# Kernel tuning notes

Measured on AMD Instinct MI355X. Metric: run time of the kernel, lower is better.

The kernel has to match this reference:

```python
import jax, jax.numpy as jnp
import numpy as np

N = 100000      # nodes
E = 1600000     # edges
IN = 256        # in_channels
H = 128         # hidden_channels
OUT = 64        # output_channels
B = 64          # graphs in batch
EPS = 1e-5      # BatchNorm eps


def setup_inputs() -> dict:
    key = jax.random.key(0)
    ks = jax.random.split(key, 32)

    def lin_w(k, fan_in, fan_out):
        return (jax.random.normal(k, (fan_in, fan_out), jnp.float32) / np.sqrt(fan_in)).astype(jnp.float32)

    inp = {
        'x': jax.random.normal(ks[0], (N, IN), jnp.float32),
        'edge_index': jax.random.randint(ks[1], (2, E), 0, N, dtype=jnp.int32),
        'batch': jnp.sort(jax.random.randint(ks[2], (N,), 0, B, dtype=jnp.int32)),
        # GCN conv weights (layer 0: IN->H, layers 1,2: H->H)
        'W0': lin_w(ks[3], IN, H), 'b0': jnp.zeros((H,), jnp.float32),
        'W1': lin_w(ks[4], H, H),  'b1': jnp.zeros((H,), jnp.float32),
        'W2': lin_w(ks[5], H, H),  'b2': jnp.zeros((H,), jnp.float32),
        # BatchNorm affine params per layer
        'g0': 1.0 + 0.1 * jax.random.normal(ks[6], (H,), jnp.float32),
        'be0': 0.1 * jax.random.normal(ks[7], (H,), jnp.float32),
        'g1': 1.0 + 0.1 * jax.random.normal(ks[8], (H,), jnp.float32),
        'be1': 0.1 * jax.random.normal(ks[9], (H,), jnp.float32),
        'g2': 1.0 + 0.1 * jax.random.normal(ks[10], (H,), jnp.float32),
        'be2': 0.1 * jax.random.normal(ks[11], (H,), jnp.float32),
        # residual projection (in_channels != hidden_channels)
        'Wres': lin_w(ks[12], IN, H), 'bres': jnp.zeros((H,), jnp.float32),
        # head MLP: Linear(H,H) -> ReLU -> Dropout(eval) -> Linear(H,OUT)
        'Wl0': lin_w(ks[13], H, H), 'bl0': jnp.zeros((H,), jnp.float32),
        'Wl1': lin_w(ks[14], H, OUT), 'bl1': jnp.zeros((OUT,), jnp.float32),
    }
    return inp


def _gcn_layer(h, src, dst, dinv, W, b):
    # PyG GCNConv: linear first, then sym-normalized aggregation with self loops
    h = h @ W                                   # [N, d_out]
    enorm = dinv[src] * dinv[dst]               # [E]
    msg = h[src] * enorm[:, None]               # gather + scale  [E, d_out]
    agg = jax.ops.segment_sum(msg, dst, num_segments=N)
    agg = agg + h * (dinv * dinv)[:, None]      # self-loop contribution (norm = 1/deg)
    return agg + b


def _bn_eval(h, g, be):
    # inference BatchNorm with running_mean=0, running_var=1
    return h * (g / np.sqrt(1.0 + EPS)) + be


def reference(x, edge_index, batch,
              W0, b0, W1, b1, W2, b2,
              g0, be0, g1, be1, g2, be2,
              Wres, bres, Wl0, bl0, Wl1, bl1):
    src, dst = edge_index[0], edge_index[1]
    # degrees with self loops (edge weight 1)
    deg = jax.ops.segment_sum(jnp.ones((E,), jnp.float32), dst, num_segments=N) + 1.0
    dinv = jax.lax.rsqrt(deg)                   # [N]

    Ws, bs, gs, bes = [W0, W1, W2], [b0, b1, b2], [g0, g1, g2], [be0, be1, be2]
    h = x
    for i in range(3):
        h = _gcn_layer(h, src, dst, dinv, Ws[i], bs[i])
        h = jax.nn.relu(_bn_eval(h, gs[i], bes[i]))  # dropout is identity in eval
        if i == 0:
            h = h + (x @ Wres + bres)           # residual projection of original input

    # head MLP on node features
    out = jax.nn.relu(h @ Wl0 + bl0) @ Wl1 + bl1    # [N, OUT]

    # global mean pool over graphs
    counts = jax.ops.segment_sum(jnp.ones((N,), jnp.float32), batch, num_segments=B)
    pooled = jax.ops.segment_sum(h, batch, num_segments=B) / jnp.maximum(counts, 1.0)[:, None]
    return out, pooled
```

## Files before the change

kernel.cpp:

```cpp
#include <hip/hip_runtime.h>
#include <hip/hip_fp16.h>

typedef __half f16;
typedef _Float16 half8 __attribute__((ext_vector_type(8)));
typedef float floatx4 __attribute__((ext_vector_type(4)));

#define NN   100000
#define NE   1600000
#define CIN  256
#define CH   128
#define COUT 64
#define NB   64

#define NBUK 128
#define NPB  782
#define BCAP 32
#define CAPB 20480
#define G1   512
#define EPB  3125
#define CSZ  15104

__global__ void k_sentinel(float* __restrict__ out, int n, float val) {
    int i = blockIdx.x * 256 + threadIdx.x;
    if (i < n) out[i] = val;
}

__global__ void k_init(float* __restrict__ pool, float* __restrict__ cnt,
                       int* __restrict__ gcur) {
    int i = blockIdx.x * 256 + threadIdx.x;
    if (i < NB * CH) pool[i] = 0.0f;
    if (i < NB) cnt[i] = 0.0f;
    if (i < NBUK) gcur[i] = i * CAPB;
}

__global__ __launch_bounds__(256) void k_bin(const int* __restrict__ src,
                                             const int* __restrict__ dst,
                                             int* __restrict__ gcur,
                                             int* __restrict__ stage) {
    __shared__ int bins[NBUK][BCAP];
    __shared__ int bcnt[NBUK];
    __shared__ int fcnt[NBUK];
    __shared__ int fbase[NBUK];
    const int tid = threadIdx.x;
    if (tid < NBUK) bcnt[tid] = 0;
    __syncthreads();
    const int e0 = blockIdx.x * EPB;
    const int e1 = (e0 + EPB < NE) ? e0 + EPB : NE;
    for (int base = e0; base < e1; base += 256) {
        int e = base + tid;
        if (e < e1) {
            int s = src[e], d = dst[e];
            int bk = d / NPB;
            int pk = ((d - bk * NPB) << 17) | s;
            int pos = atomicAdd(&bcnt[bk], 1);
            if (pos < BCAP) {
                bins[bk][pos] = pk;
            } else {
                int gp = atomicAdd(&gcur[bk], 1);
                if (gp < (bk + 1) * CAPB) stage[gp] = pk;
            }
        }
        __syncthreads();
        if (tid < NBUK) {
            int stored = bcnt[tid]; if (stored > BCAP) stored = BCAP;
            int nf = stored & ~15;
            fcnt[tid] = nf;
            if (nf) fbase[tid] = atomicAdd(&gcur[tid], nf);
        }
        __syncthreads();
#pragma unroll
        for (int pass = 0; pass < NBUK / 16; ++pass) {
            int b = pass * 16 + (tid >> 4);
            int sl = tid & 15;
            int nf = fcnt[b];
            int fb = fbase[b];
            for (int k = sl; k < nf; k += 16)
                if (fb + k < (b + 1) * CAPB) stage[fb + k] = bins[b][k];
        }
        __syncthreads();
        if (tid < NBUK) {
            int stored = bcnt[tid]; if (stored > BCAP) stored = BCAP;
            int nf = fcnt[tid];
            for (int k = nf; k < stored; ++k) bins[tid][k - nf] = bins[tid][k];
            bcnt[tid] = stored - nf;
        }
        __syncthreads();
    }
    if (tid < NBUK) {
        int stored = bcnt[tid];
        fcnt[tid] = stored;
        if (stored) fbase[tid] = atomicAdd(&gcur[tid], stored);
    }
    __syncthreads();
#pragma unroll
    for (int pass = 0; pass < NBUK / 16; ++pass) {
        int b = pass * 16 + (tid >> 4);
        int sl = tid & 15;
        int nf = fcnt[b];
        int fb = fbase[b];
        for (int k = sl; k < nf; k += 16)
            if (fb + k < (b + 1) * CAPB) stage[fb + k] = bins[b][k];
    }
}

__global__ void k_gtot(const int* __restrict__ gcur, int* __restrict__ barr,
                       int* __restrict__ rowptr) {
    int lane = threadIdx.x;
    int carry = 0;
    for (int c0 = 0; c0 < NBUK; c0 += 64) {
        int idx = c0 + lane;
        int orig = gcur[idx] - idx * CAPB;
        int v = orig;
#pragma unroll
        for (int off = 1; off < 64; off <<= 1) {
            int t = __shfl_up(v, off);
            if (lane >= off) v += t;
        }
        barr[idx] = v - orig + carry;
        carry += __shfl(v, 63);
    }
    if (lane == 0) rowptr[NN] = NE;
}

__global__ __launch_bounds__(256) void k_csr(const int* __restrict__ gcur,
                                             const int* __restrict__ barr,
                                             const int* __restrict__ stage,
                                             int* __restrict__ rowptr,
                                             int* __restrict__ csr,
                                             float* __restrict__ dinv) {
    __shared__ int hist[NPB];
    __shared__ int lcsr[CSZ];
    const int b = blockIdx.x, tid = threadIdx.x;
    const int nbase = b * NPB;
    const int nloc = (NPB < NN - nbase) ? NPB : NN - nbase;
    const int count = gcur[b] - b * CAPB;
    const int gbase = barr[b];
    const int sb = b * CAPB;
    for (int i = tid; i < NPB; i += 256) hist[i] = 0;
    __syncthreads();
    for (int i = tid; i < count; i += 256)
        atomicAdd(&hist[stage[sb + i] >> 17], 1);
    __syncthreads();
    for (int dl = tid; dl < nloc; dl += 256)
        dinv[nbase + dl] = rsqrtf((float)hist[dl] + 1.0f);
    __syncthreads();
    if (tid < 64) {
        int carry = 0;
        for (int c0 = 0; c0 < NPB; c0 += 64) {
            int idx = c0 + tid;
            int orig = (idx < NPB) ? hist[idx] : 0;
            int v = orig;
#pragma unroll
            for (int off = 1; off < 64; off <<= 1) {
                int t = __shfl_up(v, off);
                if (tid >= off) v += t;
            }
            if (idx < NPB) hist[idx] = v - orig + carry;
            carry += __shfl(v, 63);
        }
    }
    __syncthreads();
    for (int dl = tid; dl < nloc; dl += 256)
        rowptr[nbase + dl] = gbase + hist[dl];
    __syncthreads();
    const bool fits = (count <= CSZ);
    for (int i = tid; i < count; i += 256) {
        int pk = stage[sb + i];
        int dl = pk >> 17, s = pk & 0x1FFFF;
        int pos = atomicAdd(&hist[dl], 1);
        if (fits) lcsr[pos] = s;
        else csr[gbase + pos] = s;
    }
    __syncthreads();
    if (fits)
        for (int i = tid; i < count; i += 256) csr[gbase + i] = lcsr[i];
}

__global__ __launch_bounds__(256) void k_wconv(
        const float* __restrict__ W0, const float* __restrict__ Wres,
        const float* __restrict__ W1, const float* __restrict__ W2,
        const float* __restrict__ Wl0, const float* __restrict__ Wl1,
        half8* __restrict__ F0, half8* __restrict__ Fres,
        half8* __restrict__ F1, half8* __restrict__ F2,
        half8* __restrict__ Fl0, half8* __restrict__ Fl1) {
    int f = blockIdx.x * 256 + threadIdx.x;
    const float* W; half8* F; int M, base;
    if      (f <  4096) { W = W0;   F = F0;   M = 128; base = 0; }
    else if (f <  8192) { W = Wres; F = Fres; M = 128; base = 4096; }
    else if (f < 10240) { W = W1;   F = F1;   M = 128; base = 8192; }
    else if (f < 12288) { W = W2;   F = F2;   M = 128; base = 10240; }
    else if (f < 14336) { W = Wl0;  F = Fl0;  M = 128; base = 12288; }
    else if (f < 15360) { W = Wl1;  F = Fl1;  M = 64;  base = 14336; }
    else return;
    int fl = f - base;
    int lane = fl & 63, fm = lane & 15, g = lane >> 4;
    int rest = fl >> 6;
    int nt = M / 16;
    int t = rest % nt, kt = rest / nt;
    half8 v;
#pragma unroll
    for (int j = 0; j < 8; ++j)
        v[j] = (_Float16)W[(size_t)(kt * 32 + g * 8 + j) * M + t * 16 + fm];
    F[fl] = v;
}

__global__ __launch_bounds__(256) void k_mfma0(const float* __restrict__ x,
                                               const half8* __restrict__ WF,
                                               const half8* __restrict__ WFb,
                                               const float* __restrict__ bres,
                                               const float* __restrict__ dinv,
                                               f16* __restrict__ lout,
                                               f16* __restrict__ rout) {
    constexpr int APAD = 40;
    __shared__ __align__(16) _Float16 Al[2][64 * APAD];
    __shared__ __align__(16) _Float16 Bl[2][16 * 512];
    const int tid = threadIdx.x;
    const int wave = tid >> 6, lane = tid & 63;
    const int fm = lane & 15, g = lane >> 4;
    const int rb = blockIdx.x * 64;

    const int arow = tid >> 2;
    const int koff = (tid & 3) * 8;
    const int grow = rb + arow;
    const bool live = (grow < NN);
    const float* xp = x + (size_t)(live ? grow : 0) * CIN + koff;

    const int bt = wave * 4;

    floatx4 acc[16];
#pragma unroll
    for (int t = 0; t < 16; ++t)
#pragma unroll
        for (int r = 0; r < 4; ++r) acc[t][r] = 0.0f;

    float4 a0, a1;
    half8 rB[4];

    auto ldA = [&](int kt) {
        if (live) {
            a0 = *(const float4*)(xp + kt * 32);
            a1 = *(const float4*)(xp + kt * 32 + 4);
        } else {
            a0 = make_float4(0.f, 0.f, 0.f, 0.f);
            a1 = make_float4(0.f, 0.f, 0.f, 0.f);
        }
    };
    auto ldB = [&](int kt) {
#pragma unroll
        for (int i = 0; i < 4; ++i) {
            int t = bt + i;
            rB[i] = (t < 8) ? WF[((size_t)kt * 8 + t) * 64 + lane]
                            : WFb[((size_t)kt * 8 + (t - 8)) * 64 + lane];
        }
    };
    auto stA = [&](int buf) {
        half8 h;
        h[0] = (_Float16)a0.x; h[1] = (_Float16)a0.y;
        h[2] = (_Float16)a0.z; h[3] = (_Float16)a0.w;
        h[4] = (_Float16)a1.x; h[5] = (_Float16)a1.y;
        h[6] = (_Float16)a1.z; h[7] = (_Float16)a1.w;
        *(half8*)&Al[buf][arow * APAD + koff] = h;
    };
    auto stB = [&](int buf) {
#pragma unroll
        for (int i = 0; i < 4; ++i)
            *(half8*)&Bl[buf][(bt + i) * 512 + lane * 8] = rB[i];
    };

    ldA(0); ldB(0);
    stA(0); stB(0);
    __syncthreads();

    for (int kt = 0; kt < 8; ++kt) {
        const int cur = kt & 1;
        if (kt < 7) { ldA(kt + 1); ldB(kt + 1); }
        half8 afrag = *(const half8*)&Al[cur][(wave * 16 + fm) * APAD + g * 8];
#pragma unroll
        for (int t = 0; t < 8; ++t) {
            half8 bfrag = *(const half8*)&Bl[cur][t * 512 + lane * 8];
            acc[t] = __builtin_amdgcn_mfma_f32_16x16x32_f16(afrag, bfrag, acc[t], 0, 0, 0);
        }
#pragma unroll
        for (int t = 0; t < 8; ++t) {
            half8 bfrag = *(const half8*)&Bl[cur][(8 + t) * 512 + lane * 8];
            acc[8 + t] = __builtin_amdgcn_mfma_f32_16x16x32_f16(afrag, bfrag, acc[8 + t], 0, 0, 0);
        }
        if (kt < 7) { stA(cur ^ 1); stB(cur ^ 1); }
        __syncthreads();
    }

    const int rloc = wave * 16 + g * 4;
#pragma unroll
    for (int t = 0; t < 8; ++t) {
        int col = t * 16 + fm;
#pragma unroll
        for (int r = 0; r < 4; ++r) {
            int row = rb + rloc + r;
            if (row < NN) lout[(size_t)row * 128 + col] = (f16)(acc[t][r] * dinv[row]);
        }
    }
#pragma unroll
    for (int t = 0; t < 8; ++t) {
        int col = t * 16 + fm;
        float bb = bres[col];
#pragma unroll
        for (int r = 0; r < 4; ++r) {
            int row = rb + rloc + r;
            if (row < NN) rout[(size_t)row * 128 + col] = (f16)(acc[8 + t][r] + bb);
        }
    }
}

__global__ __launch_bounds__(256) void k_lin(const f16* __restrict__ A,
                                             const half8* __restrict__ WF,
                                             const float* __restrict__ dinv,
                                             f16* __restrict__ lout) {
    const int tid = threadIdx.x;
    const int wave = tid >> 6, lane = tid & 63;
    const int fm = lane & 15, g = lane >> 4;
    const int tb = blockIdx.x * 64 + wave * 16;
    const int arow = tb + fm;

    half8 af[4];
#pragma unroll
    for (int kt = 0; kt < 4; ++kt) {
        if (arow < NN) {
            af[kt] = *(const half8*)((const _Float16*)A + (size_t)arow * CH + kt * 32 + g * 8);
        } else {
#pragma unroll
            for (int i = 0; i < 8; ++i) af[kt][i] = (_Float16)0.0f;
        }
    }

    floatx4 acc[8];
#pragma unroll
    for (int t = 0; t < 8; ++t)
#pragma unroll
        for (int r = 0; r < 4; ++r) acc[t][r] = 0.0f;

#pragma unroll
    for (int kt = 0; kt < 4; ++kt)
#pragma unroll
        for (int t = 0; t < 8; ++t)
            acc[t] = __builtin_amdgcn_mfma_f32_16x16x32_f16(
                af[kt], WF[((size_t)kt * 8 + t) * 64 + lane], acc[t], 0, 0, 0);

#pragma unroll
    for (int t = 0; t < 8; ++t) {
        int col = t * 16 + fm;
#pragma unroll
        for (int r = 0; r < 4; ++r) {
            int row = tb + g * 4 + r;
            if (row < NN) lout[(size_t)row * CH + col] = (f16)(acc[t][r] * dinv[row]);
        }
    }
}

__global__ __launch_bounds__(256) void k_head(const f16* __restrict__ A,
                                              const half8* __restrict__ WF0,
                                              const half8* __restrict__ WF1,
                                              const float* __restrict__ bl0,
                                              const float* __restrict__ bl1,
                                              float* __restrict__ outp) {
    constexpr int LP = 136;
    __shared__ __align__(16) _Float16 Hs[64 * LP];
    const int tid = threadIdx.x;
    const int wave = tid >> 6, lane = tid & 63;
    const int fm = lane & 15, g = lane >> 4;
    const int tb = blockIdx.x * 64 + wave * 16;
    const int arow = tb + fm;

    half8 af[4];
#pragma unroll
    for (int kt = 0; kt < 4; ++kt) {
        if (arow < NN) {
            af[kt] = *(const half8*)((const _Float16*)A + (size_t)arow * CH + kt * 32 + g * 8);
        } else {
#pragma unroll
            for (int i = 0; i < 8; ++i) af[kt][i] = (_Float16)0.0f;
        }
    }

    floatx4 acc[8];
#pragma unroll
    for (int t = 0; t < 8; ++t)
#pragma unroll
        for (int r = 0; r < 4; ++r) acc[t][r] = 0.0f;

#pragma unroll
    for (int kt = 0; kt < 4; ++kt)
#pragma unroll
        for (int t = 0; t < 8; ++t)
            acc[t] = __builtin_amdgcn_mfma_f32_16x16x32_f16(
                af[kt], WF0[((size_t)kt * 8 + t) * 64 + lane], acc[t], 0, 0, 0);

    const int lrow = wave * 16 + g * 4;
#pragma unroll
    for (int t = 0; t < 8; ++t) {
        int col = t * 16 + fm;
        float b = bl0[col];
#pragma unroll
        for (int r = 0; r < 4; ++r)
            Hs[(lrow + r) * LP + col] = (_Float16)fmaxf(acc[t][r] + b, 0.0f);
    }
    __syncthreads();

    floatx4 acc2[4];
#pragma unroll
    for (int t = 0; t < 4; ++t)
#pragma unroll
        for (int r = 0; r < 4; ++r) acc2[t][r] = 0.0f;

#pragma unroll
    for (int kt = 0; kt < 4; ++kt) {
        half8 a2 = *(const half8*)&Hs[(wave * 16 + fm) * LP + kt * 32 + g * 8];
#pragma unroll
        for (int t = 0; t < 4; ++t)
            acc2[t] = __builtin_amdgcn_mfma_f32_16x16x32_f16(
                a2, WF1[((size_t)kt * 4 + t) * 64 + lane], acc2[t], 0, 0, 0);
    }

#pragma unroll
    for (int t = 0; t < 4; ++t) {
        int col = t * 16 + fm;
        float b = bl1[col];
#pragma unroll
        for (int r = 0; r < 4; ++r) {
            int row = tb + g * 4 + r;
            if (row < NN) outp[(size_t)row * COUT + col] = acc2[t][r] + b;
        }
    }
}

template <bool RES>
__global__ __launch_bounds__(256) void k_gather(const int* __restrict__ rowptr,
                                                const int* __restrict__ csr,
                                                const float* __restrict__ dinv,
                                                const f16* __restrict__ lin,
                                                const f16* __restrict__ res,
                                                f16* __restrict__ h,
                                                const float* __restrict__ b,
                                                const float* __restrict__ g,
                                                const float* __restrict__ be) {
    const int gw = (blockIdx.x * 256 + threadIdx.x) >> 6;
    const int lane = threadIdx.x & 63;
    if (gw >= NN) return;
    const __half2* lp = (const __half2*)lin;
    const int start = __builtin_amdgcn_readfirstlane(rowptr[gw]);
    const int end   = __builtin_amdgcn_readfirstlane(rowptr[gw + 1]);

    float2 acc = __half22float2(lp[(size_t)gw * 64 + lane]);
    int j = start;
    for (; j + 7 < end; j += 8) {
        int s0 = csr[j],     s1 = csr[j + 1], s2 = csr[j + 2], s3 = csr[j + 3];
        int s4 = csr[j + 4], s5 = csr[j + 5], s6 = csr[j + 6], s7 = csr[j + 7];
        float2 v0 = __half22float2(lp[(size_t)s0 * 64 + lane]);
        float2 v1 = __half22float2(lp[(size_t)s1 * 64 + lane]);
        float2 v2 = __half22float2(lp[(size_t)s2 * 64 + lane]);
        float2 v3 = __half22float2(lp[(size_t)s3 * 64 + lane]);
        float2 v4 = __half22float2(lp[(size_t)s4 * 64 + lane]);
        float2 v5 = __half22float2(lp[(size_t)s5 * 64 + lane]);
        float2 v6 = __half22float2(lp[(size_t)s6 * 64 + lane]);
        float2 v7 = __half22float2(lp[(size_t)s7 * 64 + lane]);
        acc.x += ((v0.x + v1.x) + (v2.x + v3.x)) + ((v4.x + v5.x) + (v6.x + v7.x));
        acc.y += ((v0.y + v1.y) + (v2.y + v3.y)) + ((v4.y + v5.y) + (v6.y + v7.y));
    }
    for (; j + 3 < end; j += 4) {
        int s0 = csr[j], s1 = csr[j + 1], s2 = csr[j + 2], s3 = csr[j + 3];
        float2 v0 = __half22float2(lp[(size_t)s0 * 64 + lane]);
        float2 v1 = __half22float2(lp[(size_t)s1 * 64 + lane]);
        float2 v2 = __half22float2(lp[(size_t)s2 * 64 + lane]);
        float2 v3 = __half22float2(lp[(size_t)s3 * 64 + lane]);
        acc.x += (v0.x + v1.x) + (v2.x + v3.x);
        acc.y += (v0.y + v1.y) + (v2.y + v3.y);
    }
    for (; j < end; ++j) {
        int s = csr[j];
        float2 v = __half22float2(lp[(size_t)s * 64 + lane]);
        acc.x += v.x;
        acc.y += v.y;
    }
    const float inv_sqrt = 0.99999500003749968f;
    float dv = dinv[gw];
    int f = lane * 2;
    float2 bb = *(const float2*)&b[f];
    float2 gg = *(const float2*)&g[f];
    float2 ee = *(const float2*)&be[f];
    float t0 = fmaxf((acc.x * dv + bb.x) * (gg.x * inv_sqrt) + ee.x, 0.0f);
    float t1 = fmaxf((acc.y * dv + bb.y) * (gg.y * inv_sqrt) + ee.y, 0.0f);
    if (RES) {
        float2 rv = __half22float2(((const __half2*)res)[(size_t)gw * 64 + lane]);
        t0 += rv.x;
        t1 += rv.y;
    }
    ((__half2*)h)[(size_t)gw * 64 + lane] = __floats2half2_rn(t0, t1);
}

__global__ void k_count(const int* __restrict__ batch, float* __restrict__ cnt) {
    __shared__ float hist[NB];
    int tid = threadIdx.x;
    if (tid < NB) hist[tid] = 0.0f;
    __syncthreads();
    int n = blockIdx.x * 256 + tid;
    if (n < NN) atomicAdd(&hist[batch[n]], 1.0f);
    __syncthreads();
    if (tid < NB && hist[tid] != 0.0f) atomicAdd(&cnt[tid], hist[tid]);
}

__global__ void k_pool(const f16* __restrict__ h, const int* __restrict__ batch,
                       float* __restrict__ pool) {
    int n0 = blockIdx.x * 64;
    int j = threadIdx.x;
    int cur = batch[n0];
    float acc = 0.0f;
    int nend = (n0 + 64 < NN) ? n0 + 64 : NN;
    for (int n = n0; n < nend; ++n) {
        int b = batch[n];
        if (b != cur) {
            atomicAdd(&pool[cur * CH + j], acc);
            acc = 0.0f;
            cur = b;
        }
        acc += (float)h[(size_t)n * CH + j];
    }
    atomicAdd(&pool[cur * CH + j], acc);
}

__global__ void k_pool_fin(const float* __restrict__ pool,
                           const float* __restrict__ cnt,
                           float* __restrict__ out) {
    int i = blockIdx.x * 256 + threadIdx.x;
    if (i < NB * CH) {
        float c = fmaxf(cnt[i / CH], 1.0f);
        out[i] = pool[i] / c;
    }
}

extern "C" void kernel_launch(void* const* d_in, const int* in_sizes, int n_in,
                              void* d_out, int out_size, void* d_ws, size_t ws_size,
                              hipStream_t stream) {
    float* outp  = (float*)d_out;
    float* poolp = outp + (size_t)NN * COUT;

    const size_t HB = (size_t)NN * CH * 2;
    const size_t LB = (size_t)NN * CH * 2;
    const size_t RB = (size_t)NN * CH * 2;
    const size_t DV = (size_t)NN * 4;
    const size_t RP = 400016;
    const size_t CS = (size_t)NE * 4;
    const size_t GC = 512;
    const size_t BA = 528;
    const size_t PL = (size_t)NB * CH * 4;
    const size_t CT = 256;
    const size_t F0B = 4096 * 16, F1B = 2048 * 16, FLB = 1024 * 16;
    const size_t need = HB + LB + RB + DV + RP + CS + GC + BA + PL + CT
                        + 2 * F0B + 3 * F1B + FLB;
    if (ws_size < need) {
        k_sentinel<<<(out_size + 255) / 256, 256, 0, stream>>>(outp, out_size, 2000.0f);
        return;
    }
    char* p = (char*)d_ws;
    f16*   hbuf   = (f16*)p;               p += HB;
    f16*   lbuf   = (f16*)p;               p += LB;
    f16*   rbuf   = (f16*)p;
    int*   stage  = (int*)p;               p += RB;
    float* dinv   = (float*)p;             p += DV;
    int*   rowptr = (int*)p;               p += RP;
    int*   csr    = (int*)p;               p += CS;
    int*   gcur   = (int*)p;               p += GC;
    int*   barr   = (int*)p;               p += BA;
    float* pool   = (float*)p;             p += PL;
    float* cnt    = (float*)p;             p += CT;
    half8* F0     = (half8*)p;             p += F0B;
    half8* Fres   = (half8*)p;             p += F0B;
    half8* F1     = (half8*)p;             p += F1B;
    half8* F2     = (half8*)p;             p += F1B;
    half8* Fl0    = (half8*)p;             p += F1B;
    half8* Fl1    = (half8*)p;

    const float* x   = (const float*)d_in[0];
    const int*   ei  = (const int*)d_in[1];
    const int*   bat = (const int*)d_in[2];
    const float* W0 = (const float*)d_in[3],  *b0 = (const float*)d_in[4];
    const float* W1 = (const float*)d_in[5],  *b1 = (const float*)d_in[6];
    const float* W2 = (const float*)d_in[7],  *b2 = (const float*)d_in[8];
    const float* g0 = (const float*)d_in[9],  *be0 = (const float*)d_in[10];
    const float* g1 = (const float*)d_in[11], *be1 = (const float*)d_in[12];
    const float* g2 = (const float*)d_in[13], *be2 = (const float*)d_in[14];
    const float* Wres = (const float*)d_in[15], *bres = (const float*)d_in[16];
    const float* Wl0 = (const float*)d_in[17], *bl0 = (const float*)d_in[18];
    const float* Wl1 = (const float*)d_in[19], *bl1 = (const float*)d_in[20];

    const int* src = ei;
    const int* dst = ei + NE;

    const int gRow = (NN + 63) / 64;
    const int gGat = (NN * 64) / 256;

    k_init<<<33, 256, 0, stream>>>(pool, cnt, gcur);
    k_wconv<<<60, 256, 0, stream>>>(W0, Wres, W1, W2, Wl0, Wl1,
                                    F0, Fres, F1, F2, Fl0, Fl1);
    k_bin<<<G1, 256, 0, stream>>>(src, dst, gcur, stage);
    k_gtot<<<1, 64, 0, stream>>>(gcur, barr, rowptr);
    k_csr<<<NBUK, 256, 0, stream>>>(gcur, barr, stage, rowptr, csr, dinv);

    k_mfma0<<<gRow, 256, 0, stream>>>(x, F0, Fres, bres, dinv, lbuf, rbuf);
    k_gather<true><<<gGat, 256, 0, stream>>>(rowptr, csr, dinv, lbuf, rbuf, hbuf, b0, g0, be0);

    k_lin<<<gRow, 256, 0, stream>>>(hbuf, F1, dinv, lbuf);
    k_gather<false><<<gGat, 256, 0, stream>>>(rowptr, csr, dinv, lbuf, nullptr, hbuf, b1, g1, be1);

    k_lin<<<gRow, 256, 0, stream>>>(hbuf, F2, dinv, lbuf);
    k_gather<false><<<gGat, 256, 0, stream>>>(rowptr, csr, dinv, lbuf, nullptr, hbuf, b2, g2, be2);

    k_count<<<(NN + 255) / 256, 256, 0, stream>>>(bat, cnt);
    k_pool<<<gRow, 128, 0, stream>>>(hbuf, bat, pool);
    k_pool_fin<<<(NB * CH + 255) / 256, 256, 0, stream>>>(pool, cnt, poolp);

    k_head<<<gRow, 256, 0, stream>>>(hbuf, Fl0, Fl1, bl0, bl1, outp);
}
```

Before: 640.1 us.

## Build CSR with global atomic degree count and atomic-cursor fill instead of bucket binning

Replaces the two-pass bucket-binning CSR construction (shared-memory bins, staging buffer, per-bucket local sort) with a plain counting sort. Degrees come from global atomics, a per-bucket sum and scan produce row pointers, and edges are scattered into the CSR through global atomic cursors. This removes the staging buffer traffic and the heavy shared-memory bin management, at the cost of many contended global atomics and random scattered writes. The resulting per-row neighbor order is nondeterministic, which could change the locality of the later gathers.

```diff
diff --git a/kernel.cpp b/kernel.cpp
--- a/kernel.cpp
+++ b/kernel.cpp
@@ -14,11 +14,6 @@
 
 #define NBUK 128
 #define NPB  782
-#define BCAP 32
-#define CAPB 20480
-#define G1   512
-#define EPB  3125
-#define CSZ  15104
 
 __global__ void k_sentinel(float* __restrict__ out, int n, float val) {
     int i = blockIdx.x * 256 + threadIdx.x;
@@ -26,90 +21,47 @@
 }
 
 __global__ void k_init(float* __restrict__ pool, float* __restrict__ cnt,
-                       int* __restrict__ gcur) {
+                       int* __restrict__ deg) {
     int i = blockIdx.x * 256 + threadIdx.x;
     if (i < NB * CH) pool[i] = 0.0f;
     if (i < NB) cnt[i] = 0.0f;
-    if (i < NBUK) gcur[i] = i * CAPB;
-}
-
-__global__ __launch_bounds__(256) void k_bin(const int* __restrict__ src,
-                                             const int* __restrict__ dst,
-                                             int* __restrict__ gcur,
-                                             int* __restrict__ stage) {
-    __shared__ int bins[NBUK][BCAP];
-    __shared__ int bcnt[NBUK];
-    __shared__ int fcnt[NBUK];
-    __shared__ int fbase[NBUK];
-    const int tid = threadIdx.x;
-    if (tid < NBUK) bcnt[tid] = 0;
-    __syncthreads();
-    const int e0 = blockIdx.x * EPB;
-    const int e1 = (e0 + EPB < NE) ? e0 + EPB : NE;
-    for (int base = e0; base < e1; base += 256) {
-        int e = base + tid;
-        if (e < e1) {
-            int s = src[e], d = dst[e];
-            int bk = d / NPB;
-            int pk = ((d - bk * NPB) << 17) | s;
-            int pos = atomicAdd(&bcnt[bk], 1);
-            if (pos < BCAP) {
-                bins[bk][pos] = pk;
-            } else {
-                int gp = atomicAdd(&gcur[bk], 1);
-                if (gp < (bk + 1) * CAPB) stage[gp] = pk;
-            }
-        }
-        __syncthreads();
-        if (tid < NBUK) {
-            int stored = bcnt[tid]; if (stored > BCAP) stored = BCAP;
-            int nf = stored & ~15;
-            fcnt[tid] = nf;
-            if (nf) fbase[tid] = atomicAdd(&gcur[tid], nf);
-        }
-        __syncthreads();
-#pragma unroll
-        for (int pass = 0; pass < NBUK / 16; ++pass) {
-            int b = pass * 16 + (tid >> 4);
-            int sl = tid & 15;
-            int nf = fcnt[b];
-            int fb = fbase[b];
-            for (int k = sl; k < nf; k += 16)
-                if (fb + k < (b + 1) * CAPB) stage[fb + k] = bins[b][k];
-        }
-        __syncthreads();
-        if (tid < NBUK) {
-            int stored = bcnt[tid]; if (stored > BCAP) stored = BCAP;
-            int nf = fcnt[tid];
-            for (int k = nf; k < stored; ++k) bins[tid][k - nf] = bins[tid][k];
-            bcnt[tid] = stored - nf;
-        }
-        __syncthreads();
-    }
-    if (tid < NBUK) {
-        int stored = bcnt[tid];
-        fcnt[tid] = stored;
-        if (stored) fbase[tid] = atomicAdd(&gcur[tid], stored);
-    }
-    __syncthreads();
-#pragma unroll
-    for (int pass = 0; pass < NBUK / 16; ++pass) {
-        int b = pass * 16 + (tid >> 4);
-        int sl = tid & 15;
-        int nf = fcnt[b];
-        int fb = fbase[b];
-        for (int k = sl; k < nf; k += 16)
-            if (fb + k < (b + 1) * CAPB) stage[fb + k] = bins[b][k];
-    }
-}
-
-__global__ void k_gtot(const int* __restrict__ gcur, int* __restrict__ barr,
-                       int* __restrict__ rowptr) {
+    if (i < NN) deg[i] = 0;
+}
+
+__global__ __launch_bounds__(256) void k_deg(const int* __restrict__ dst,
+                                             int* __restrict__ deg) {
+    int i = blockIdx.x * 256 + threadIdx.x;
+    if (i < NE / 4) {
+        int4 d = ((const int4*)dst)[i];
+        atomicAdd(&deg[d.x], 1);
+        atomicAdd(&deg[d.y], 1);
+        atomicAdd(&deg[d.z], 1);
+        atomicAdd(&deg[d.w], 1);
+    }
+}
+
+__global__ __launch_bounds__(256) void k_bsum(const int* __restrict__ deg,
+                                              int* __restrict__ bsum) {
+    __shared__ int red[4];
+    const int b = blockIdx.x, tid = threadIdx.x;
+    const int nbase = b * NPB;
+    const int nend = (nbase + NPB < NN) ? nbase + NPB : NN;
+    int s = 0;
+    for (int i = nbase + tid; i < nend; i += 256) s += deg[i];
+#pragma unroll
+    for (int off = 32; off; off >>= 1) s += __shfl_down(s, off);
+    if ((tid & 63) == 0) red[tid >> 6] = s;
+    __syncthreads();
+    if (tid == 0) bsum[b] = red[0] + red[1] + red[2] + red[3];
+}
+
+__global__ void k_scanb(const int* __restrict__ bsum, int* __restrict__ barr,
+                        int* __restrict__ rowptr) {
     int lane = threadIdx.x;
     int carry = 0;
     for (int c0 = 0; c0 < NBUK; c0 += 64) {
         int idx = c0 + lane;
-        int orig = gcur[idx] - idx * CAPB;
+        int orig = bsum[idx];
         int v = orig;
 #pragma unroll
         for (int off = 1; off < 64; off <<= 1) {
@@ -122,24 +74,16 @@
     if (lane == 0) rowptr[NN] = NE;
 }
 
-__global__ __launch_bounds__(256) void k_csr(const int* __restrict__ gcur,
-                                             const int* __restrict__ barr,
-                                             const int* __restrict__ stage,
-                                             int* __restrict__ rowptr,
-                                             int* __restrict__ csr,
-                                             float* __restrict__ dinv) {
+__global__ __launch_bounds__(256) void k_brow(const int* __restrict__ deg,
+                                              const int* __restrict__ barr,
+                                              int* __restrict__ rowptr,
+                                              int* __restrict__ cursor,
+                                              float* __restrict__ dinv) {
     __shared__ int hist[NPB];
-    __shared__ int lcsr[CSZ];
     const int b = blockIdx.x, tid = threadIdx.x;
     const int nbase = b * NPB;
     const int nloc = (NPB < NN - nbase) ? NPB : NN - nbase;
-    const int count = gcur[b] - b * CAPB;
-    const int gbase = barr[b];
-    const int sb = b * CAPB;
-    for (int i = tid; i < NPB; i += 256) hist[i] = 0;
-    __syncthreads();
-    for (int i = tid; i < count; i += 256)
-        atomicAdd(&hist[stage[sb + i] >> 17], 1);
+    for (int i = tid; i < nloc; i += 256) hist[i] = deg[nbase + i];
     __syncthreads();
     for (int dl = tid; dl < nloc; dl += 256)
         dinv[nbase + dl] = rsqrtf((float)hist[dl] + 1.0f);
@@ -148,7 +92,7 @@
         int carry = 0;
         for (int c0 = 0; c0 < NPB; c0 += 64) {
             int idx = c0 + tid;
-            int orig = (idx < NPB) ? hist[idx] : 0;
+            int orig = (idx < nloc) ? hist[idx] : 0;
             int v = orig;
 #pragma unroll
             for (int off = 1; off < 64; off <<= 1) {
@@ -160,20 +104,27 @@
         }
     }
     __syncthreads();
-    for (int dl = tid; dl < nloc; dl += 256)
-        rowptr[nbase + dl] = gbase + hist[dl];
-    __syncthreads();
-    const bool fits = (count <= CSZ);
-    for (int i = tid; i < count; i += 256) {
-        int pk = stage[sb + i];
-        int dl = pk >> 17, s = pk & 0x1FFFF;
-        int pos = atomicAdd(&hist[dl], 1);
-        if (fits) lcsr[pos] = s;
-        else csr[gbase + pos] = s;
-    }
-    __syncthreads();
-    if (fits)
-        for (int i = tid; i < count; i += 256) csr[gbase + i] = lcsr[i];
+    const int gbase = barr[b];
+    for (int dl = tid; dl < nloc; dl += 256) {
+        int rp = gbase + hist[dl];
+        rowptr[nbase + dl] = rp;
+        cursor[nbase + dl] = rp;
+    }
+}
+
+__global__ __launch_bounds__(256) void k_fill(const int* __restrict__ src,
+                                              const int* __restrict__ dst,
+                                              int* __restrict__ cursor,
+                                              int* __restrict__ csr) {
+    int i = blockIdx.x * 256 + threadIdx.x;
+    if (i < NE / 4) {
+        int4 s = ((const int4*)src)[i];
+        int4 d = ((const int4*)dst)[i];
+        int p0 = atomicAdd(&cursor[d.x], 1); csr[p0] = s.x;
+        int p1 = atomicAdd(&cursor[d.y], 1); csr[p1] = s.y;
+        int p2 = atomicAdd(&cursor[d.z], 1); csr[p2] = s.z;
+        int p3 = atomicAdd(&cursor[d.w], 1); csr[p3] = s.w;
+    }
 }
 
 __global__ __launch_bounds__(256) void k_wconv(
@@ -563,11 +514,13 @@
     f16*   hbuf   = (f16*)p;               p += HB;
     f16*   lbuf   = (f16*)p;               p += LB;
     f16*   rbuf   = (f16*)p;
-    int*   stage  = (int*)p;               p += RB;
+    int*   deg    = (int*)p;
+    int*   cursor = (int*)p + 100096;
+    p += RB;
     float* dinv   = (float*)p;             p += DV;
     int*   rowptr = (int*)p;               p += RP;
     int*   csr    = (int*)p;               p += CS;
-    int*   gcur   = (int*)p;               p += GC;
+    int*   bsum   = (int*)p;               p += GC;
     int*   barr   = (int*)p;               p += BA;
     float* pool   = (float*)p;             p += PL;
     float* cnt    = (float*)p;             p += CT;
@@ -596,13 +549,16 @@
 
     const int gRow = (NN + 63) / 64;
     const int gGat = (NN * 64) / 256;
-
-    k_init<<<33, 256, 0, stream>>>(pool, cnt, gcur);
+    const int gE4  = (NE / 4 + 255) / 256;
+
+    k_init<<<(NN + 255) / 256, 256, 0, stream>>>(pool, cnt, deg);
     k_wconv<<<60, 256, 0, stream>>>(W0, Wres, W1, W2, Wl0, Wl1,
                                     F0, Fres, F1, F2, Fl0, Fl1);
-    k_bin<<<G1, 256, 0, stream>>>(src, dst, gcur, stage);
-    k_gtot<<<1, 64, 0, stream>>>(gcur, barr, rowptr);
-    k_csr<<<NBUK, 256, 0, stream>>>(gcur, barr, stage, rowptr, csr, dinv);
+    k_deg<<<gE4, 256, 0, stream>>>(dst, deg);
+    k_bsum<<<NBUK, 256, 0, stream>>>(deg, bsum);
+    k_scanb<<<1, 64, 0, stream>>>(bsum, barr, rowptr);
+    k_brow<<<NBUK, 256, 0, stream>>>(deg, barr, rowptr, cursor, dinv);
+    k_fill<<<gE4, 256, 0, stream>>>(src, dst, cursor, csr);
 
     k_mfma0<<<gRow, 256, 0, stream>>>(x, F0, Fres, bres, dinv, lbuf, rbuf);
     k_gather<true><<<gGat, 256, 0, stream>>>(rowptr, csr, dinv, lbuf, rbuf, hbuf, b0, g0, be0);
```

New measurement: 723.5 us. +13.0%, slower.
